# Optimization experiments

Measured on AMD Instinct MI355X. Metric: run time of the kernel, lower is better.

The kernel has to match this reference:

```python
import jax, jax.numpy as jnp
import numpy as np

N = 1024
IN_F = 256
OUT_F = 128
H = 4
NH = OUT_F // H  # 32
NEG_SLOPE = 0.2


def setup_inputs() -> dict:
    key = jax.random.key(0)
    k1, k2, k3, k4, k5 = jax.random.split(key, 5)
    h = jax.random.normal(k1, (N, IN_F), dtype=jnp.float32)
    adj_mat = jax.random.randint(k2, (N, N, 1), 0, 2, dtype=jnp.int32)
    s_in = 1.0 / np.sqrt(IN_F)
    s_nh = 1.0 / np.sqrt(NH)
    Wl = jax.random.uniform(k3, (H * NH, IN_F), jnp.float32, -s_in, s_in)
    Wr = jax.random.uniform(k4, (H * NH, IN_F), jnp.float32, -s_in, s_in)
    attn_w = jax.random.uniform(k5, (NH,), jnp.float32, -s_nh, s_nh)
    return {"h": h, "adj_mat": adj_mat, "Wl": Wl, "Wr": Wr, "attn_w": attn_w}


def reference(h, adj_mat, Wl, Wr, attn_w):
    n = h.shape[0]
    g_l = (h @ Wl.T).reshape(n, H, NH)  # [N,H,F]
    g_r = (h @ Wr.T).reshape(n, H, NH)  # [N,H,F]
    # g_sum[i, j] = g_l[j] + g_r[i]  (repeat / repeat_interleave semantics)
    g_sum = g_l[None, :, :, :] + g_r[:, None, :, :]  # [N,N,H,F]
    act = jnp.where(g_sum >= 0, g_sum, NEG_SLOPE * g_sum)
    e = jnp.einsum('ijhf,f->ijh', act, attn_w)  # [N,N,H]
    mask = adj_mat != 0  # [N,N,1] broadcasts over heads
    e = jnp.where(mask, e, -jnp.inf)
    a = jax.nn.softmax(e, axis=1)  # softmax over source nodes j
    h_prime = jnp.einsum('ijh,jhf->ihf', a, g_r).reshape(n, H * NH)
    # is_output_layer=False -> ELU (dropout is a no-op in eval)
    return jax.nn.elu(h_prime)
```

## Files before the change

kernel.cpp:

```cpp
#include <hip/hip_runtime.h>
#include <math.h>

#define NN 1024
#define IN_F 256
#define OUT_F 128
#define NHEADS 4
#define NHF 32
#define HPSTR 260

__global__ void __launch_bounds__(256) glr_gemm(const float* __restrict__ hmat,
                                                const float* __restrict__ Wl,
                                                const float* __restrict__ Wr,
                                                float* __restrict__ glh,
                                                float* __restrict__ grh) {
    __shared__ float hp[64 * HPSTR];
    const int tid = threadIdx.x;
    const int rg = blockIdx.x & 15;
    const int cs = blockIdx.x >> 4;

    const float4* __restrict__ hsrc = (const float4*)hmat + rg * (64 * 64);
#pragma unroll
    for (int i = 0; i < 16; ++i) {
        const int v = tid + i * 256;
        const int row = v >> 6, kq = v & 63;
        const float4 x = hsrc[v];
        *(float4*)(hp + row * HPSTR + kq * 4) = x;
    }
    __syncthreads();

    const int lane = tid & 63;
    const int wu = __builtin_amdgcn_readfirstlane(tid >> 6);
    const int c0 = cs * 16 + wu * 4;
    const float* __restrict__ wbase = (c0 < OUT_F) ? (Wl + c0 * IN_F)
                                                   : (Wr + (c0 - OUT_F) * IN_F);
    const float* __restrict__ hrow = hp + lane * HPSTR;

    float a0 = 0.f, a1 = 0.f, a2 = 0.f, a3 = 0.f;
#pragma unroll 4
    for (int kq = 0; kq < 64; ++kq) {
        const float4 hv = *(const float4*)(hrow + kq * 4);
        const float4 w0 = *(const float4*)(wbase + 0 * IN_F + kq * 4);
        const float4 w1 = *(const float4*)(wbase + 1 * IN_F + kq * 4);
        const float4 w2 = *(const float4*)(wbase + 2 * IN_F + kq * 4);
        const float4 w3 = *(const float4*)(wbase + 3 * IN_F + kq * 4);
        a0 = fmaf(hv.x, w0.x, fmaf(hv.y, w0.y, fmaf(hv.z, w0.z, fmaf(hv.w, w0.w, a0))));
        a1 = fmaf(hv.x, w1.x, fmaf(hv.y, w1.y, fmaf(hv.z, w1.z, fmaf(hv.w, w1.w, a1))));
        a2 = fmaf(hv.x, w2.x, fmaf(hv.y, w2.y, fmaf(hv.z, w2.z, fmaf(hv.w, w2.w, a2))));
        a3 = fmaf(hv.x, w3.x, fmaf(hv.y, w3.y, fmaf(hv.z, w3.z, fmaf(hv.w, w3.w, a3))));
    }

    const int row = rg * 64 + lane;
    const int cb = c0 & (OUT_F - 1);
    const int hh = cb >> 5;
    const int f  = cb & 31;
    float* __restrict__ dst = (c0 < OUT_F) ? glh : grh;
    float4 r; r.x = a0; r.y = a1; r.z = a2; r.w = a3;
    *(float4*)(dst + (hh * NN + row) * NHF + f) = r;
}

__global__ void __launch_bounds__(512) gat_main(const float* __restrict__ glh,
                                                const float* __restrict__ grh,
                                                const int* __restrict__ adj,
                                                const float* __restrict__ attn_w,
                                                float* __restrict__ out) {
    const int hh  = blockIdx.y;
    const int i0  = blockIdx.x * 8;
    const int tid = threadIdx.x;

    __shared__ float p_buf[8][1028];
    __shared__ float part[8][32][34];
    __shared__ float red[8][8];
    __shared__ float l_sh[8];

    float lpart[8];
#pragma unroll
    for (int ii = 0; ii < 8; ++ii) lpart[ii] = 0.f;

    for (int c = 0; c < 2; ++c) {
        const int j = (c << 9) + tid;
        const float* __restrict__ gp = glh + (hh * NN + j) * NHF;
        float gl[NHF];
#pragma unroll
        for (int f4 = 0; f4 < 8; ++f4) {
            const float4 v = *(const float4*)(gp + (f4 << 2));
            gl[4 * f4 + 0] = v.x; gl[4 * f4 + 1] = v.y;
            gl[4 * f4 + 2] = v.z; gl[4 * f4 + 3] = v.w;
        }
        float alpha = 0.f;
#pragma unroll
        for (int f = 0; f < NHF; ++f) alpha = fmaf(gl[f], attn_w[f], alpha);
        int adjv[8];
#pragma unroll
        for (int ii = 0; ii < 8; ++ii) adjv[ii] = adj[(i0 + ii) * NN + j];
#pragma unroll
        for (int ii = 0; ii < 8; ++ii) {
            const float* __restrict__ grp = grh + (hh * NN + i0 + ii) * NHF;
            float S0 = 0.f, S1 = 0.f;
#pragma unroll
            for (int f = 0; f < NHF; f += 2) {
                const float s0 = gl[f]     + grp[f];
                const float s1 = gl[f + 1] + grp[f + 1];
                S0 = fmaf(fabsf(s0), attn_w[f],     S0);
                S1 = fmaf(fabsf(s1), attn_w[f + 1], S1);
            }
            const float e = fmaf(0.4f, S0 + S1, 0.6f * alpha);
            const float p = adjv[ii] ? __expf(e) : 0.f;
            p_buf[ii][j] = p;
            lpart[ii] += p;
        }
    }

    const int lane = tid & 63, wv = tid >> 6;
#pragma unroll
    for (int ii = 0; ii < 8; ++ii) {
        float v = lpart[ii];
#pragma unroll
        for (int d = 32; d > 0; d >>= 1) v += __shfl_xor(v, d);
        if (lane == 0) red[ii][wv] = v;
    }
    __syncthreads();
    if (tid < 8) {
        float l = red[tid][0];
#pragma unroll
        for (int w = 1; w < 8; ++w) l += red[tid][w];
        l_sh[tid] = l;
    }
    __syncthreads();

    const int fs = tid & 15;
    const int js = tid >> 4;
    const int rot = (js & 3) << 3;
    const float* __restrict__ gp = grh + hh * NN * NHF + (fs << 1);
    float o0[8], o1[8];
#pragma unroll
    for (int ii = 0; ii < 8; ++ii) { o0[ii] = 0.f; o1[ii] = 0.f; }
    const int jb = js << 5;
    for (int jj = 0; jj < 32; jj += 4) {
        const int j = jb + ((jj + rot) & 31);
        const float2 g0 = *(const float2*)(gp + (j + 0) * NHF);
        const float2 g1 = *(const float2*)(gp + (j + 1) * NHF);
        const float2 g2 = *(const float2*)(gp + (j + 2) * NHF);
        const float2 g3 = *(const float2*)(gp + (j + 3) * NHF);
#pragma unroll
        for (int ii = 0; ii < 8; ++ii) {
            const float4 p4 = *(const float4*)&p_buf[ii][j];
            o0[ii] = fmaf(p4.x, g0.x, fmaf(p4.y, g1.x, fmaf(p4.z, g2.x, fmaf(p4.w, g3.x, o0[ii]))));
            o1[ii] = fmaf(p4.x, g0.y, fmaf(p4.y, g1.y, fmaf(p4.z, g2.y, fmaf(p4.w, g3.y, o1[ii]))));
        }
    }
#pragma unroll
    for (int ii = 0; ii < 8; ++ii) {
        float2 t; t.x = o0[ii]; t.y = o1[ii];
        *(float2*)&part[ii][js][fs << 1] = t;
    }
    __syncthreads();

    if (tid < 256) {
        const int ii = tid >> 5, ff = tid & 31;
        float s0 = 0.f, s1 = 0.f, s2 = 0.f, s3 = 0.f;
#pragma unroll
        for (int k = 0; k < 32; k += 4) {
            s0 += part[ii][k + 0][ff];
            s1 += part[ii][k + 1][ff];
            s2 += part[ii][k + 2][ff];
            s3 += part[ii][k + 3][ff];
        }
        float s = (s0 + s1) + (s2 + s3);
        s /= l_sh[ii];
        const float r = (s > 0.f) ? s : (__expf(s) - 1.f);
        out[(i0 + ii) * OUT_F + hh * NHF + ff] = r;
    }
}

extern "C" void kernel_launch(void* const* d_in, const int* in_sizes, int n_in,
                              void* d_out, int out_size, void* d_ws, size_t ws_size,
                              hipStream_t stream) {
    const float* hmat = (const float*)d_in[0];
    const int*   adj  = (const int*)d_in[1];
    const float* Wl   = (const float*)d_in[2];
    const float* Wr   = (const float*)d_in[3];
    const float* aw   = (const float*)d_in[4];
    float* o          = (float*)d_out;

    float* glh = (float*)d_ws;
    float* grh = glh + NHEADS * NN * NHF;

    glr_gemm<<<dim3(256), dim3(256), 0, stream>>>(hmat, Wl, Wr, glh, grh);
    gat_main<<<dim3(NN / 8, NHEADS), dim3(512), 0, stream>>>(glh, grh, adj, aw, o);
}
```

Baseline: 111.4 us.

## Halve row tile per block, add warp-shuffle reduction and split accumulators

Reduces the number of destination rows per block from 8 to 4, doubling the grid so more blocks are in flight, and adds a min-blocks launch bound. The cross-thread partial-sum reduction is changed to use wavefront shuffles before writing to shared memory, which shrinks the shared partial buffer and the final reduction loop. The per-row dot products are also split into four independent accumulators to shorten FMA dependency chains. The trade-off is that each block recomputes alpha and reloads g_l for fewer rows, so total g_l reads and alpha work double.

```diff
diff --git a/kernel.cpp b/kernel.cpp
--- a/kernel.cpp
+++ b/kernel.cpp
@@ -6,6 +6,7 @@
 #define OUT_F 128
 #define NHEADS 4
 #define NHF 32
+#define ITILE 4
 #define HPSTR 260
 
 __global__ void __launch_bounds__(256) glr_gemm(const float* __restrict__ hmat,
@@ -58,24 +59,25 @@
     *(float4*)(dst + (hh * NN + row) * NHF + f) = r;
 }
 
-__global__ void __launch_bounds__(512) gat_main(const float* __restrict__ glh,
-                                                const float* __restrict__ grh,
-                                                const int* __restrict__ adj,
-                                                const float* __restrict__ attn_w,
-                                                float* __restrict__ out) {
+__global__ void __launch_bounds__(512, 8) gat_main(const float* __restrict__ glh,
+                                                   const float* __restrict__ grh,
+                                                   const int* __restrict__ adj,
+                                                   const float* __restrict__ attn_w,
+                                                   float* __restrict__ out) {
     const int hh  = blockIdx.y;
-    const int i0  = blockIdx.x * 8;
+    const int i0  = blockIdx.x * ITILE;
     const int tid = threadIdx.x;
 
-    __shared__ float p_buf[8][1028];
-    __shared__ float part[8][32][34];
-    __shared__ float red[8][8];
-    __shared__ float l_sh[8];
-
-    float lpart[8];
-#pragma unroll
-    for (int ii = 0; ii < 8; ++ii) lpart[ii] = 0.f;
-
+    __shared__ float p_buf[ITILE][1028];
+    __shared__ float part[ITILE][8][34];
+    __shared__ float red[ITILE][8];
+    __shared__ float l_sh[ITILE];
+
+    float lpart[ITILE];
+#pragma unroll
+    for (int ii = 0; ii < ITILE; ++ii) lpart[ii] = 0.f;
+
+#pragma unroll 1
     for (int c = 0; c < 2; ++c) {
         const int j = (c << 9) + tid;
         const float* __restrict__ gp = glh + (hh * NN + j) * NHF;
@@ -86,24 +88,34 @@
             gl[4 * f4 + 0] = v.x; gl[4 * f4 + 1] = v.y;
             gl[4 * f4 + 2] = v.z; gl[4 * f4 + 3] = v.w;
         }
-        float alpha = 0.f;
-#pragma unroll
-        for (int f = 0; f < NHF; ++f) alpha = fmaf(gl[f], attn_w[f], alpha);
-        int adjv[8];
-#pragma unroll
-        for (int ii = 0; ii < 8; ++ii) adjv[ii] = adj[(i0 + ii) * NN + j];
-#pragma unroll
-        for (int ii = 0; ii < 8; ++ii) {
+        float al0 = 0.f, al1 = 0.f, al2 = 0.f, al3 = 0.f;
+#pragma unroll
+        for (int f = 0; f < NHF; f += 4) {
+            al0 = fmaf(gl[f + 0], attn_w[f + 0], al0);
+            al1 = fmaf(gl[f + 1], attn_w[f + 1], al1);
+            al2 = fmaf(gl[f + 2], attn_w[f + 2], al2);
+            al3 = fmaf(gl[f + 3], attn_w[f + 3], al3);
+        }
+        const float alpha = (al0 + al1) + (al2 + al3);
+        int adjv[ITILE];
+#pragma unroll
+        for (int ii = 0; ii < ITILE; ++ii) adjv[ii] = adj[(i0 + ii) * NN + j];
+#pragma unroll
+        for (int ii = 0; ii < ITILE; ++ii) {
             const float* __restrict__ grp = grh + (hh * NN + i0 + ii) * NHF;
-            float S0 = 0.f, S1 = 0.f;
-#pragma unroll
-            for (int f = 0; f < NHF; f += 2) {
-                const float s0 = gl[f]     + grp[f];
+            float S0 = 0.f, S1 = 0.f, S2 = 0.f, S3 = 0.f;
+#pragma unroll
+            for (int f = 0; f < NHF; f += 4) {
+                const float s0 = gl[f + 0] + grp[f + 0];
                 const float s1 = gl[f + 1] + grp[f + 1];
-                S0 = fmaf(fabsf(s0), attn_w[f],     S0);
+                const float s2 = gl[f + 2] + grp[f + 2];
+                const float s3 = gl[f + 3] + grp[f + 3];
+                S0 = fmaf(fabsf(s0), attn_w[f + 0], S0);
                 S1 = fmaf(fabsf(s1), attn_w[f + 1], S1);
+                S2 = fmaf(fabsf(s2), attn_w[f + 2], S2);
+                S3 = fmaf(fabsf(s3), attn_w[f + 3], S3);
             }
-            const float e = fmaf(0.4f, S0 + S1, 0.6f * alpha);
+            const float e = fmaf(0.4f, (S0 + S1) + (S2 + S3), 0.6f * alpha);
             const float p = adjv[ii] ? __expf(e) : 0.f;
             p_buf[ii][j] = p;
             lpart[ii] += p;
@@ -112,14 +124,14 @@
 
     const int lane = tid & 63, wv = tid >> 6;
 #pragma unroll
-    for (int ii = 0; ii < 8; ++ii) {
+    for (int ii = 0; ii < ITILE; ++ii) {
         float v = lpart[ii];
 #pragma unroll
         for (int d = 32; d > 0; d >>= 1) v += __shfl_xor(v, d);
         if (lane == 0) red[ii][wv] = v;
     }
     __syncthreads();
-    if (tid < 8) {
+    if (tid < ITILE) {
         float l = red[tid][0];
 #pragma unroll
         for (int w = 1; w < 8; ++w) l += red[tid][w];
@@ -131,9 +143,9 @@
     const int js = tid >> 4;
     const int rot = (js & 3) << 3;
     const float* __restrict__ gp = grh + hh * NN * NHF + (fs << 1);
-    float o0[8], o1[8];
-#pragma unroll
-    for (int ii = 0; ii < 8; ++ii) { o0[ii] = 0.f; o1[ii] = 0.f; }
+    float o0[ITILE], o1[ITILE];
+#pragma unroll
+    for (int ii = 0; ii < ITILE; ++ii) { o0[ii] = 0.f; o1[ii] = 0.f; }
     const int jb = js << 5;
     for (int jj = 0; jj < 32; jj += 4) {
         const int j = jb + ((jj + rot) & 31);
@@ -142,31 +154,37 @@
         const float2 g2 = *(const float2*)(gp + (j + 2) * NHF);
         const float2 g3 = *(const float2*)(gp + (j + 3) * NHF);
 #pragma unroll
-        for (int ii = 0; ii < 8; ++ii) {
+        for (int ii = 0; ii < ITILE; ++ii) {
             const float4 p4 = *(const float4*)&p_buf[ii][j];
             o0[ii] = fmaf(p4.x, g0.x, fmaf(p4.y, g1.x, fmaf(p4.z, g2.x, fmaf(p4.w, g3.x, o0[ii]))));
             o1[ii] = fmaf(p4.x, g0.y, fmaf(p4.y, g1.y, fmaf(p4.z, g2.y, fmaf(p4.w, g3.y, o1[ii]))));
         }
     }
 #pragma unroll
-    for (int ii = 0; ii < 8; ++ii) {
-        float2 t; t.x = o0[ii]; t.y = o1[ii];
-        *(float2*)&part[ii][js][fs << 1] = t;
-    }
-    __syncthreads();
-
-    if (tid < 256) {
+    for (int ii = 0; ii < ITILE; ++ii) {
+        o0[ii] += __shfl_xor(o0[ii], 16);
+        o0[ii] += __shfl_xor(o0[ii], 32);
+        o1[ii] += __shfl_xor(o1[ii], 16);
+        o1[ii] += __shfl_xor(o1[ii], 32);
+    }
+    if (lane < 16) {
+#pragma unroll
+        for (int ii = 0; ii < ITILE; ++ii) {
+            float2 t; t.x = o0[ii]; t.y = o1[ii];
+            *(float2*)&part[ii][wv][fs << 1] = t;
+        }
+    }
+    __syncthreads();
+
+    if (tid < 32 * ITILE) {
         const int ii = tid >> 5, ff = tid & 31;
-        float s0 = 0.f, s1 = 0.f, s2 = 0.f, s3 = 0.f;
-#pragma unroll
-        for (int k = 0; k < 32; k += 4) {
-            s0 += part[ii][k + 0][ff];
-            s1 += part[ii][k + 1][ff];
-            s2 += part[ii][k + 2][ff];
-            s3 += part[ii][k + 3][ff];
-        }
-        float s = (s0 + s1) + (s2 + s3);
-        s /= l_sh[ii];
+        float s0 = 0.f, s1 = 0.f;
+#pragma unroll
+        for (int w = 0; w < 8; w += 2) {
+            s0 += part[ii][w + 0][ff];
+            s1 += part[ii][w + 1][ff];
+        }
+        float s = (s0 + s1) / l_sh[ii];
         const float r = (s > 0.f) ? s : (__expf(s) - 1.f);
         out[(i0 + ii) * OUT_F + hh * NHF + ff] = r;
     }
@@ -186,5 +204,5 @@
     float* grh = glh + NHEADS * NN * NHF;
 
     glr_gemm<<<dim3(256), dim3(256), 0, stream>>>(hmat, Wl, Wr, glh, grh);
-    gat_main<<<dim3(NN / 8, NHEADS), dim3(512), 0, stream>>>(glh, grh, adj, aw, o);
+    gat_main<<<dim3(NN / ITILE, NHEADS), dim3(512), 0, stream>>>(glh, grh, adj, aw, o);
 }
```

After: 106.9 us. -4.1%, faster.
